# Optimization experiments

Hardware: AMD Instinct MI355X
Metric: run time of the kernel (lower is better)

The kernel has to match this reference:

```python
import jax, jax.numpy as jnp
import numpy as np

CH = 512
RED = CH // 8  # 64


def setup_inputs() -> dict:
    key = jax.random.key(0)
    ks = jax.random.split(key, 8)
    s = 0.05
    x = jax.random.normal(ks[0], (4, CH, 64, 64), dtype=jnp.float32)
    Wq = jax.random.normal(ks[1], (RED, CH), dtype=jnp.float32) * s
    bq = jnp.zeros((RED,), dtype=jnp.float32)
    Wk = jax.random.normal(ks[2], (RED, CH), dtype=jnp.float32) * s
    bk = jnp.zeros((RED,), dtype=jnp.float32)
    Wv = jax.random.normal(ks[3], (CH, CH), dtype=jnp.float32) * s
    bv = jnp.zeros((CH,), dtype=jnp.float32)
    gamma = jnp.zeros((1,), dtype=jnp.float32)
    return {"x": x, "Wq": Wq, "bq": bq, "Wk": Wk, "bk": bk, "Wv": Wv, "bv": bv, "gamma": gamma}


def reference(x, Wq, bq, Wk, bk, Wv, bv, gamma):
    b, c, h, w = x.shape
    n = h * w
    xf = x.reshape(b, c, n)  # [b, c, n]
    # 1x1 convs == per-pixel linear over channels
    q = jnp.einsum('rc,bcn->bnr', Wq, xf) + bq[None, None, :]   # [b, n, red]
    k = jnp.einsum('rc,bcn->brn', Wk, xf) + bk[None, :, None]   # [b, red, n]
    v = jnp.einsum('oc,bcn->bon', Wv, xf) + bv[None, :, None]   # [b, c, n]
    energy = jnp.einsum('bnr,brm->bnm', q, k)                   # [b, n, n]
    attention = jax.nn.softmax(energy, axis=-1)
    # out[b,c,i] = sum_j v[b,c,j] * attention[b,i,j]
    out = jnp.einsum('bcj,bij->bci', v, attention).reshape(b, c, h, w)
    return gamma[0] * out + x
```

## Files before the change

### kernel.cpp

```cpp
#include <hip/hip_runtime.h>
#include <math.h>

#define CH 512
#define RED 64

typedef __attribute__((ext_vector_type(4))) float f32x4;
typedef long i64;

typedef const __attribute__((address_space(1))) void* gas_t;
typedef __attribute__((address_space(3))) void* las_t;

static __device__ __forceinline__ void gl16(const void* g, void* l) {
    __builtin_amdgcn_global_load_lds((gas_t)g, (las_t)l, 16, 0, 0);
}

static __device__ __forceinline__ unsigned pk4(float a, float b, float c, float d) {
    int w = __builtin_amdgcn_cvt_pk_fp8_f32(a, b, 0, false);
    w = __builtin_amdgcn_cvt_pk_fp8_f32(c, d, w, true);
    return (unsigned)w;
}
static __device__ __forceinline__ unsigned char pk1(float a) {
    return (unsigned char)(__builtin_amdgcn_cvt_pk_fp8_f32(a, a, 0, false) & 0xFF);
}

__global__ __launch_bounds__(128) void prep_w(
    const float* __restrict__ Wq, const float* __restrict__ Wk,
    const float* __restrict__ Wv, unsigned char* __restrict__ Wcat)
{
    const int r = blockIdx.x, t = threadIdx.x;
    const float* src = (r < 64) ? (Wq + (size_t)r * CH)
                     : (r < 128) ? (Wk + (size_t)(r - 64) * CH)
                                 : (Wv + (size_t)(r - 128) * CH);
    const float4 v = *(const float4*)&src[t * 4];
    *(unsigned*)&Wcat[(size_t)r * CH + t * 4] = pk4(v.x, v.y, v.z, v.w);
}

__global__ __launch_bounds__(256) void cast_xt(
    const float* __restrict__ x, unsigned char* __restrict__ xT, int n)
{
    __shared__ float sX[64][65];
    const int b = blockIdx.z, i0 = blockIdx.x * 64, c0 = blockIdx.y * 64;
    const int t = threadIdx.x;
    #pragma unroll
    for (int s = 0; s < 4; ++s) {
        const int id = s * 256 + t, c = id >> 4, seg = id & 15;
        *(float4*)&sX[c][seg * 4] = *(const float4*)&x[((size_t)b * CH + c0 + c) * n + i0 + seg * 4];
    }
    __syncthreads();
    const int i = t >> 2, cp = t & 3;
    uint4 w;
    w.x = pk4(sX[cp*16+ 0][i], sX[cp*16+ 1][i], sX[cp*16+ 2][i], sX[cp*16+ 3][i]);
    w.y = pk4(sX[cp*16+ 4][i], sX[cp*16+ 5][i], sX[cp*16+ 6][i], sX[cp*16+ 7][i]);
    w.z = pk4(sX[cp*16+ 8][i], sX[cp*16+ 9][i], sX[cp*16+10][i], sX[cp*16+11][i]);
    w.w = pk4(sX[cp*16+12][i], sX[cp*16+13][i], sX[cp*16+14][i], sX[cp*16+15][i]);
    *(uint4*)&xT[((size_t)b * n + i0 + i) * CH + c0 + cp * 16] = w;
}

__global__ __launch_bounds__(256, 4) void qkv_gemm(
    const unsigned char* __restrict__ xT, const unsigned char* __restrict__ Wcat,
    const float* __restrict__ bq, const float* __restrict__ bk,
    const float* __restrict__ bv,
    unsigned char* __restrict__ qF, unsigned char* __restrict__ kF,
    unsigned char* __restrict__ v2, int n)
{
    __shared__ char smem[20480];
    const int b = blockIdx.z, i0 = blockIdx.x * 128, o0 = blockIdx.y * 128;
    const int t = threadIdx.x, lane = t & 63;
    const int quad = lane >> 4, l16 = lane & 15;
    const int wrow = (t >> 6) & 1, wcol = t >> 7;

    f32x4 acc[4][4];
    const f32x4 zz = {0.f, 0.f, 0.f, 0.f};
    #pragma unroll
    for (int mi = 0; mi < 4; ++mi)
        #pragma unroll
        for (int ci = 0; ci < 4; ++ci) acc[mi][ci] = zz;

    const unsigned char* Ab = xT + ((size_t)b * n + i0) * CH;
    const unsigned char* Bb = Wcat + (size_t)o0 * CH;

    for (int c0 = 0; c0 < CH; c0 += 64) {
        #pragma unroll
        for (int s = 0; s < 5; ++s) {
            const int c = s * 256 + t;
            const bool isA = c < 640;
            const int tc = isA ? c : c - 640;
            const int r = tc / 5, p = (tc % 5) & 3;
            gl16((isA ? Ab : Bb) + (size_t)r * CH + c0 + p * 16,
                 smem + (isA ? 0 : 10240) + (size_t)tc * 16);
        }
        __syncthreads();
        #pragma unroll
        for (int kk = 0; kk < 64; kk += 32) {
            i64 af[4], bf[4];
            #pragma unroll
            for (int mi = 0; mi < 4; ++mi)
                af[mi] = *(const i64*)(smem + (wrow * 64 + mi * 16 + l16) * 80 + kk + quad * 8);
            #pragma unroll
            for (int ci = 0; ci < 4; ++ci)
                bf[ci] = *(const i64*)(smem + 10240 + (wcol * 64 + ci * 16 + l16) * 80 + kk + quad * 8);
            #pragma unroll
            for (int mi = 0; mi < 4; ++mi)
                #pragma unroll
                for (int ci = 0; ci < 4; ++ci)
                    acc[mi][ci] = __builtin_amdgcn_mfma_f32_16x16x32_fp8_fp8(af[mi], bf[ci], acc[mi][ci], 0, 0, 0);
        }
        __syncthreads();
    }

    float bb[4];
    #pragma unroll
    for (int ci = 0; ci < 4; ++ci) {
        const int o = wcol * 64 + ci * 16 + l16;
        bb[ci] = (o0 == 0) ? ((o < 64) ? bq[o] : bk[o - 64]) : bv[o0 - 128 + o];
    }
    __syncthreads();
    unsigned char* sE = (unsigned char*)smem;
    if (o0 == 0) {
        #pragma unroll
        for (int mi = 0; mi < 4; ++mi)
            #pragma unroll
            for (int ci = 0; ci < 4; ++ci)
                #pragma unroll
                for (int r = 0; r < 4; ++r)
                    sE[(wrow*64 + mi*16 + quad*4 + r) * 144 + wcol*64 + ci*16 + l16] =
                        pk1(acc[mi][ci][r] + bb[ci]);
    } else {
        #pragma unroll
        for (int mi = 0; mi < 4; ++mi)
            #pragma unroll
            for (int ci = 0; ci < 4; ++ci)
                #pragma unroll
                for (int r = 0; r < 4; ++r)
                    sE[(wcol*64 + ci*16 + l16) * 144 + wrow*64 + mi*16 + quad*4 + r] =
                        pk1(acc[mi][ci][r] + bb[ci]);
    }
    __syncthreads();
    if (o0 == 0) {
        #pragma unroll
        for (int u = 0; u < 2; ++u) {
            const int id = u * 256 + t, i = id >> 2, p = id & 3;
            *(uint4*)&qF[((size_t)b * n + i0 + i) * RED + p * 16] = *(const uint4*)&sE[i * 144 + p * 16];
        }
        #pragma unroll
        for (int u = 0; u < 2; ++u) {
            const int id = u * 256 + t, i = id >> 2, p = id & 3;
            *(uint4*)&kF[((size_t)b * n + i0 + i) * RED + p * 16] = *(const uint4*)&sE[i * 144 + 64 + p * 16];
        }
    } else {
        #pragma unroll
        for (int u = 0; u < 4; ++u) {
            const int id = u * 256 + t, o = id >> 3, p = id & 7;
            *(uint4*)&v2[((size_t)b * CH + (o0 - 128) + o) * n + i0 + p * 16] =
                *(const uint4*)&sE[o * 144 + p * 16];
        }
    }
}

__global__ __launch_bounds__(256, 4) void rowmax(
    const unsigned char* __restrict__ qF, const unsigned char* __restrict__ kF,
    unsigned* __restrict__ mKey, int n)
{
    __shared__ char smem[20480];
    const int b = blockIdx.z, i0 = blockIdx.y * 128, j0 = blockIdx.x * 128;
    const int t = threadIdx.x, lane = t & 63;
    const int quad = lane >> 4, l16 = lane & 15;
    const int wrow = (t >> 6) & 1, wcol = t >> 7;

    const unsigned char* Qb = qF + ((size_t)b * n + i0) * RED;
    const unsigned char* Kb = kF + ((size_t)b * n + j0) * RED;
    #pragma unroll
    for (int s = 0; s < 5; ++s) {
        const int c = s * 256 + t;
        const bool isQ = c < 640;
        const int tc = isQ ? c : c - 640;
        const int r = tc / 5, p = (tc % 5) & 3;
        gl16((isQ ? Qb : Kb) + (size_t)r * RED + p * 16,
             smem + (isQ ? 0 : 10240) + (size_t)tc * 16);
    }
    __syncthreads();

    f32x4 acc[4][4];
    const f32x4 zz = {0.f, 0.f, 0.f, 0.f};
    #pragma unroll
    for (int mi = 0; mi < 4; ++mi)
        #pragma unroll
        for (int ci = 0; ci < 4; ++ci) acc[mi][ci] = zz;

    #pragma unroll
    for (int kk = 0; kk < 64; kk += 32) {
        i64 af[4], bf[4];
        #pragma unroll
        for (int mi = 0; mi < 4; ++mi)
            af[mi] = *(const i64*)(smem + (wrow * 64 + mi * 16 + l16) * 80 + kk + quad * 8);
        #pragma unroll
        for (int ci = 0; ci < 4; ++ci)
            bf[ci] = *(const i64*)(smem + 10240 + (wcol * 64 + ci * 16 + l16) * 80 + kk + quad * 8);
        #pragma unroll
        for (int mi = 0; mi < 4; ++mi)
            #pragma unroll
            for (int ci = 0; ci < 4; ++ci)
                acc[mi][ci] = __builtin_amdgcn_mfma_f32_16x16x32_fp8_fp8(af[mi], bf[ci], acc[mi][ci], 0, 0, 0);
    }

    #pragma unroll
    for (int mi = 0; mi < 4; ++mi)
        #pragma unroll
        for (int r = 0; r < 4; ++r) {
            float mx = fmaxf(fmaxf(acc[mi][0][r], acc[mi][1][r]),
                             fmaxf(acc[mi][2][r], acc[mi][3][r]));
            #pragma unroll
            for (int off = 1; off < 16; off <<= 1) mx = fmaxf(mx, __shfl_xor(mx, off));
            if (l16 == 0) {
                union { float f; unsigned u; } cv; cv.f = mx;
                const unsigned key = ((int)cv.u >= 0) ? (cv.u + 0x80000000u) : ~cv.u;
                atomicMax(&mKey[(size_t)b * n + i0 + wrow * 64 + mi * 16 + quad * 4 + r], key);
            }
        }
}

#define STGSZ 12288
#define SPOFF 24576
#define SLOFF 32768

__global__ __launch_bounds__(512, 4) void attn(
    const unsigned char* __restrict__ qF,
    const unsigned char* __restrict__ kF,
    const unsigned char* __restrict__ v2,
    const unsigned* __restrict__ mKey,
    const float* __restrict__ x, const float* __restrict__ gamma,
    float* __restrict__ y, int n)
{
    __shared__ char smem[34816];
    const int combo = blockIdx.x, it = blockIdx.y;
    const int b = combo >> 2, ch0 = (combo & 3) * 128;
    const int i0 = it * 128;
    const int t = threadIdx.x, lane = t & 63, w = t >> 6;
    const int quad = lane >> 4, l16 = lane & 15;
    const int qh = w & 1, g = w >> 1;
    const int sw = (l16 >> 1) & 3;
    const int boff = (quad & 1) * 8;
    const int phalf = quad >> 1;

    const unsigned char* Qb = qF + ((size_t)b * n + i0) * RED;
    const unsigned char* Kb = kF + (size_t)b * n * RED;
    const unsigned char* Vb = v2 + ((size_t)b * CH + ch0) * n;

    {
        const int r = t >> 2, s = t & 3, gs = s ^ ((r >> 1) & 3);
        gl16(Qb + (size_t)r * RED + gs * 16, smem + SPOFF + (size_t)t * 16);
        if (t < 256) {
            const int kr = t >> 2, ks = t & 3, kgs = ks ^ ((kr >> 1) & 3);
            gl16(Kb + (size_t)kr * RED + kgs * 16, smem + (size_t)t * 16);
        }
        gl16(Vb + (size_t)r * n + gs * 16, smem + 4096 + (size_t)t * 16);
    }
    __syncthreads();

    i64 qreg[4][2];
    #pragma unroll
    for (int qt = 0; qt < 4; ++qt) {
        const int row = qh * 64 + qt * 16 + l16;
        #pragma unroll
        for (int kki = 0; kki < 2; ++kki) {
            const int p = (kki * 2 + phalf) ^ sw;
            qreg[qt][kki] = *(const i64*)(smem + SPOFF + row * 64 + p * 16 + boff);
        }
    }
    float mrow[4];
    #pragma unroll
    for (int qt = 0; qt < 4; ++qt) {
        const unsigned u = mKey[(size_t)b * n + i0 + qh * 64 + qt * 16 + l16];
        const unsigned bits = (u >= 0x80000000u) ? (u - 0x80000000u) : ~u;
        union { unsigned u; float f; } cv; cv.u = bits;
        mrow[qt] = cv.f;
    }

    f32x4 acc[4][2];
    const f32x4 zz = {0.f, 0.f, 0.f, 0.f};
    #pragma unroll
    for (int qt = 0; qt < 4; ++qt) { acc[qt][0] = zz; acc[qt][1] = zz; }
    float lacc[4] = {0.f, 0.f, 0.f, 0.f};

    const int nchunks = n >> 6;
    for (int c = 0; c < nchunks; ++c) {
        const int j0 = c << 6;
        char* cur = smem + (c & 1) * STGSZ;
        char* nxt = smem + ((c & 1) ^ 1) * STGSZ;

        __syncthreads();
        if (j0 + 64 < n) {
            const int jn = j0 + 64;
            const int r = t >> 2, s = t & 3, gs = s ^ ((r >> 1) & 3);
            if (t < 256)
                gl16(Kb + (size_t)(jn + r) * RED + gs * 16, nxt + (size_t)t * 16);
            gl16(Vb + (size_t)r * n + jn + gs * 16, nxt + 4096 + (size_t)t * 16);
        }

        f32x4 S[4];
        #pragma unroll
        for (int qt = 0; qt < 4; ++qt) S[qt] = zz;
        #pragma unroll
        for (int kki = 0; kki < 2; ++kki) {
            const int p = (kki * 2 + phalf) ^ sw;
            const i64 kf = *(const i64*)(cur + (g * 16 + l16) * 64 + p * 16 + boff);
            #pragma unroll
            for (int qt = 0; qt < 4; ++qt)
                S[qt] = __builtin_amdgcn_mfma_f32_16x16x32_fp8_fp8(kf, qreg[qt][kki], S[qt], 0, 0, 0);
        }
        #pragma unroll
        for (int qt = 0; qt < 4; ++qt) {
            const float e0 = __expf(S[qt][0] - mrow[qt]);
            const float e1 = __expf(S[qt][1] - mrow[qt]);
            const float e2 = __expf(S[qt][2] - mrow[qt]);
            const float e3 = __expf(S[qt][3] - mrow[qt]);
            lacc[qt] += (e0 + e1) + (e2 + e3);
            const int qrow = qh * 64 + qt * 16 + l16;
            const int pp = g ^ sw;
            *(unsigned*)(smem + SPOFF + qrow * 64 + pp * 16 + quad * 4) = pk4(e0, e1, e2, e3);
        }
        __syncthreads();

        #pragma unroll
        for (int kki = 0; kki < 2; ++kki) {
            const int p = (kki * 2 + phalf) ^ sw;
            i64 vf[2], pf[4];
            #pragma unroll
            for (int ct = 0; ct < 2; ++ct) {
                const int row = (g * 2 + ct) * 16 + l16;
                vf[ct] = *(const i64*)(cur + 4096 + row * 64 + p * 16 + boff);
            }
            #pragma unroll
            for (int qt = 0; qt < 4; ++qt) {
                const int qrow = qh * 64 + qt * 16 + l16;
                pf[qt] = *(const i64*)(smem + SPOFF + qrow * 64 + p * 16 + boff);
            }
            #pragma unroll
            for (int qt = 0; qt < 4; ++qt)
                #pragma unroll
                for (int ct = 0; ct < 2; ++ct)
                    acc[qt][ct] = __builtin_amdgcn_mfma_f32_16x16x32_fp8_fp8(vf[ct], pf[qt], acc[qt][ct], 0, 0, 0);
        }
    }

    float* sL = (float*)(smem + SLOFF);
    #pragma unroll
    for (int qt = 0; qt < 4; ++qt) {
        float v = lacc[qt];
        v += __shfl_xor(v, 16);
        v += __shfl_xor(v, 32);
        lacc[qt] = v;
    }
    if (quad == 0) {
        #pragma unroll
        for (int qt = 0; qt < 4; ++qt) sL[w * 64 + qt * 16 + l16] = lacc[qt];
    }
    __syncthreads();
    float il[4];
    #pragma unroll
    for (int qt = 0; qt < 4; ++qt) {
        const int idx = qt * 16 + l16;
        il[qt] = 1.0f / (sL[qh * 64 + idx] + sL[(2 + qh) * 64 + idx] +
                         sL[(4 + qh) * 64 + idx] + sL[(6 + qh) * 64 + idx]);
    }

    const float gm = gamma[0];
    float* sT = (float*)smem;
    #pragma unroll
    for (int cr = 0; cr < 4; ++cr) {
        __syncthreads();
        if (g == cr) {
            #pragma unroll
            for (int ct = 0; ct < 2; ++ct)
                #pragma unroll
                for (int qt = 0; qt < 4; ++qt)
                    #pragma unroll
                    for (int r = 0; r < 4; ++r)
                        sT[(ct * 16 + quad * 4 + r) * 132 + qh * 64 + qt * 16 + l16] =
                            acc[qt][ct][r] * il[qt];
        }
        __syncthreads();
        const int row = t >> 4, seg = (t & 15) * 8;
        const size_t gb = ((size_t)b * CH + ch0 + cr * 32 + row) * n + i0 + seg;
        #pragma unroll
        for (int u = 0; u < 2; ++u) {
            const float4 xv = *(const float4*)&x[gb + u * 4];
            const float* op = &sT[row * 132 + seg + u * 4];
            float4 yv;
            yv.x = gm * op[0] + xv.x;
            yv.y = gm * op[1] + xv.y;
            yv.z = gm * op[2] + xv.z;
            yv.w = gm * op[3] + xv.w;
            *(float4*)&y[gb + u * 4] = yv;
        }
    }
}

extern "C" void kernel_launch(void* const* d_in, const int* in_sizes, int n_in,
                              void* d_out, int out_size, void* d_ws, size_t ws_size,
                              hipStream_t stream) {
    const float* x     = (const float*)d_in[0];
    const float* Wq    = (const float*)d_in[1];
    const float* bq    = (const float*)d_in[2];
    const float* Wk    = (const float*)d_in[3];
    const float* bk    = (const float*)d_in[4];
    const float* Wv    = (const float*)d_in[5];
    const float* bv    = (const float*)d_in[6];
    const float* gamma = (const float*)d_in[7];
    float* y = (float*)d_out;

    const int N = 64 * 64;
    const int B = in_sizes[0] / (CH * N);

    char* ws = (char*)d_ws;
    unsigned char* xT   = (unsigned char*)ws;  ws += (size_t)B * N * CH;
    unsigned char* qF   = (unsigned char*)ws;  ws += (size_t)B * N * RED;
    unsigned char* kF   = (unsigned char*)ws;  ws += (size_t)B * N * RED;
    unsigned char* v2   = (unsigned char*)ws;  ws += (size_t)B * CH * N;
    unsigned char* Wcat = (unsigned char*)ws;  ws += (size_t)640 * CH;
    unsigned* mKey      = (unsigned*)ws;

    hipMemsetAsync(mKey, 0, (size_t)B * N * 4, stream);

    prep_w<<<dim3(640), 128, 0, stream>>>(Wq, Wk, Wv, Wcat);
    cast_xt<<<dim3(N / 64, CH / 64, B), 256, 0, stream>>>(x, xT, N);
    qkv_gemm<<<dim3(N / 128, 5, B), 256, 0, stream>>>(xT, Wcat, bq, bk, bv, qF, kF, v2, N);
    rowmax<<<dim3(N / 128, N / 128, B), 256, 0, stream>>>(qF, kF, mKey, N);
    attn<<<dim3(4 * B, N / 128), 512, 0, stream>>>(qF, kF, v2, mKey, x, gamma, y, N);
}
```

Measured before the change: 253.1 us.

## Retile attention to 64 queries x 256 channels and fold log2e into Q

The attention kernel now gives each block 64 query rows and 256 output channels instead of 128x128. Each warp holds 2 query tiles and 4 channel tiles, and the staging buffers grow to hold twice as much V per chunk. This cuts the redundant QK^T and softmax work that was repeated across the four channel groups down to two groups. Q is pre-scaled by log2(e) in the projection so the softmax can use the hardware exp2 directly. The risk is that larger shared memory and more accumulators may lower occupancy, and fp8 rounding of the scaled Q slightly changes numerics.

```diff
diff --git a/kernel.cpp b/kernel.cpp
--- a/kernel.cpp
+++ b/kernel.cpp
@@ -21,6 +21,14 @@
 }
 static __device__ __forceinline__ unsigned char pk1(float a) {
     return (unsigned char)(__builtin_amdgcn_cvt_pk_fp8_f32(a, a, 0, false) & 0xFF);
+}
+
+static __device__ __forceinline__ float fexp2(float v) {
+#if __has_builtin(__builtin_amdgcn_exp2f)
+    return __builtin_amdgcn_exp2f(v);
+#else
+    float r; asm("v_exp_f32 %0, %1" : "=v"(r) : "v"(v)); return r;
+#endif
 }
 
 __global__ __launch_bounds__(128) void prep_w(
@@ -108,11 +116,17 @@
         __syncthreads();
     }
 
-    float bb[4];
+    float bb[4], scl[4];
     #pragma unroll
     for (int ci = 0; ci < 4; ++ci) {
         const int o = wcol * 64 + ci * 16 + l16;
-        bb[ci] = (o0 == 0) ? ((o < 64) ? bq[o] : bk[o - 64]) : bv[o0 - 128 + o];
+        if (o0 == 0) {
+            bb[ci]  = (o < 64) ? bq[o] : bk[o - 64];
+            scl[ci] = (o < 64) ? 1.44269504088896f : 1.0f;
+        } else {
+            bb[ci]  = bv[o0 - 128 + o];
+            scl[ci] = 1.0f;
+        }
     }
     __syncthreads();
     unsigned char* sE = (unsigned char*)smem;
@@ -124,7 +138,7 @@
                 #pragma unroll
                 for (int r = 0; r < 4; ++r)
                     sE[(wrow*64 + mi*16 + quad*4 + r) * 144 + wcol*64 + ci*16 + l16] =
-                        pk1(acc[mi][ci][r] + bb[ci]);
+                        pk1((acc[mi][ci][r] + bb[ci]) * scl[ci]);
     } else {
         #pragma unroll
         for (int mi = 0; mi < 4; ++mi)
@@ -219,9 +233,9 @@
         }
 }
 
-#define STGSZ 12288
-#define SPOFF 24576
-#define SLOFF 32768
+#define STGSZ 20480
+#define SPOFF 40960
+#define SLOFF 45056
 
 __global__ __launch_bounds__(512, 4) void attn(
     const unsigned char* __restrict__ qF,
@@ -231,10 +245,9 @@
     const float* __restrict__ x, const float* __restrict__ gamma,
     float* __restrict__ y, int n)
 {
-    __shared__ char smem[34816];
-    const int combo = blockIdx.x, it = blockIdx.y;
-    const int b = combo >> 2, ch0 = (combo & 3) * 128;
-    const int i0 = it * 128;
+    __shared__ char smem[46080];
+    const int b = blockIdx.x >> 1, ch0 = (blockIdx.x & 1) * 256;
+    const int i0 = blockIdx.y * 64;
     const int t = threadIdx.x, lane = t & 63, w = t >> 6;
     const int quad = lane >> 4, l16 = lane & 15;
     const int qh = w & 1, g = w >> 1;
@@ -248,39 +261,45 @@
 
     {
         const int r = t >> 2, s = t & 3, gs = s ^ ((r >> 1) & 3);
-        gl16(Qb + (size_t)r * RED + gs * 16, smem + SPOFF + (size_t)t * 16);
         if (t < 256) {
-            const int kr = t >> 2, ks = t & 3, kgs = ks ^ ((kr >> 1) & 3);
-            gl16(Kb + (size_t)kr * RED + kgs * 16, smem + (size_t)t * 16);
-        }
-        gl16(Vb + (size_t)r * n + gs * 16, smem + 4096 + (size_t)t * 16);
-    }
-    __syncthreads();
-
-    i64 qreg[4][2];
-    #pragma unroll
-    for (int qt = 0; qt < 4; ++qt) {
-        const int row = qh * 64 + qt * 16 + l16;
+            gl16(Qb + (size_t)r * RED + gs * 16, smem + SPOFF + (size_t)t * 16);
+            gl16(Kb + (size_t)r * RED + gs * 16, smem + (size_t)t * 16);
+        }
+        #pragma unroll
+        for (int ps = 0; ps < 2; ++ps) {
+            const int id = ps * 512 + t, vr = id >> 2, vs = id & 3;
+            const int vgs = vs ^ ((vr >> 1) & 3);
+            gl16(Vb + (size_t)vr * n + vgs * 16, smem + 4096 + (size_t)id * 16);
+        }
+    }
+    __syncthreads();
+
+    i64 qreg[2][2];
+    #pragma unroll
+    for (int qt = 0; qt < 2; ++qt) {
+        const int row = qh * 32 + qt * 16 + l16;
         #pragma unroll
         for (int kki = 0; kki < 2; ++kki) {
             const int p = (kki * 2 + phalf) ^ sw;
             qreg[qt][kki] = *(const i64*)(smem + SPOFF + row * 64 + p * 16 + boff);
         }
     }
-    float mrow[4];
-    #pragma unroll
-    for (int qt = 0; qt < 4; ++qt) {
-        const unsigned u = mKey[(size_t)b * n + i0 + qh * 64 + qt * 16 + l16];
+    float mrow[2];
+    #pragma unroll
+    for (int qt = 0; qt < 2; ++qt) {
+        const unsigned u = mKey[(size_t)b * n + i0 + qh * 32 + qt * 16 + l16];
         const unsigned bits = (u >= 0x80000000u) ? (u - 0x80000000u) : ~u;
         union { unsigned u; float f; } cv; cv.u = bits;
         mrow[qt] = cv.f;
     }
 
-    f32x4 acc[4][2];
+    f32x4 acc[2][4];
     const f32x4 zz = {0.f, 0.f, 0.f, 0.f};
     #pragma unroll
-    for (int qt = 0; qt < 4; ++qt) { acc[qt][0] = zz; acc[qt][1] = zz; }
-    float lacc[4] = {0.f, 0.f, 0.f, 0.f};
+    for (int qt = 0; qt < 2; ++qt)
+        #pragma unroll
+        for (int ct = 0; ct < 4; ++ct) acc[qt][ct] = zz;
+    float lacc[2] = {0.f, 0.f};
 
     const int nchunks = n >> 6;
     for (int c = 0; c < nchunks; ++c) {
@@ -294,28 +313,32 @@
             const int r = t >> 2, s = t & 3, gs = s ^ ((r >> 1) & 3);
             if (t < 256)
                 gl16(Kb + (size_t)(jn + r) * RED + gs * 16, nxt + (size_t)t * 16);
-            gl16(Vb + (size_t)r * n + jn + gs * 16, nxt + 4096 + (size_t)t * 16);
-        }
-
-        f32x4 S[4];
-        #pragma unroll
-        for (int qt = 0; qt < 4; ++qt) S[qt] = zz;
+            #pragma unroll
+            for (int ps = 0; ps < 2; ++ps) {
+                const int id = ps * 512 + t, vr = id >> 2, vs = id & 3;
+                const int vgs = vs ^ ((vr >> 1) & 3);
+                gl16(Vb + (size_t)vr * n + jn + vgs * 16, nxt + 4096 + (size_t)id * 16);
+            }
+        }
+
+        f32x4 S[2];
+        S[0] = zz; S[1] = zz;
         #pragma unroll
         for (int kki = 0; kki < 2; ++kki) {
             const int p = (kki * 2 + phalf) ^ sw;
             const i64 kf = *(const i64*)(cur + (g * 16 + l16) * 64 + p * 16 + boff);
             #pragma unroll
-            for (int qt = 0; qt < 4; ++qt)
+            for (int qt = 0; qt < 2; ++qt)
                 S[qt] = __builtin_amdgcn_mfma_f32_16x16x32_fp8_fp8(kf, qreg[qt][kki], S[qt], 0, 0, 0);
         }
         #pragma unroll
-        for (int qt = 0; qt < 4; ++qt) {
-            const float e0 = __expf(S[qt][0] - mrow[qt]);
-            const float e1 = __expf(S[qt][1] - mrow[qt]);
-            const float e2 = __expf(S[qt][2] - mrow[qt]);
-            const float e3 = __expf(S[qt][3] - mrow[qt]);
+        for (int qt = 0; qt < 2; ++qt) {
+            const float e0 = fexp2(S[qt][0] - mrow[qt]);
+            const float e1 = fexp2(S[qt][1] - mrow[qt]);
+            const float e2 = fexp2(S[qt][2] - mrow[qt]);
+            const float e3 = fexp2(S[qt][3] - mrow[qt]);
             lacc[qt] += (e0 + e1) + (e2 + e3);
-            const int qrow = qh * 64 + qt * 16 + l16;
+            const int qrow = qh * 32 + qt * 16 + l16;
             const int pp = g ^ sw;
             *(unsigned*)(smem + SPOFF + qrow * 64 + pp * 16 + quad * 4) = pk4(e0, e1, e2, e3);
         }
@@ -324,28 +347,28 @@
         #pragma unroll
         for (int kki = 0; kki < 2; ++kki) {
             const int p = (kki * 2 + phalf) ^ sw;
-            i64 vf[2], pf[4];
-            #pragma unroll
-            for (int ct = 0; ct < 2; ++ct) {
-                const int row = (g * 2 + ct) * 16 + l16;
+            i64 vf[4], pf[2];
+            #pragma unroll
+            for (int ct = 0; ct < 4; ++ct) {
+                const int row = g * 64 + ct * 16 + l16;
                 vf[ct] = *(const i64*)(cur + 4096 + row * 64 + p * 16 + boff);
             }
             #pragma unroll
-            for (int qt = 0; qt < 4; ++qt) {
-                const int qrow = qh * 64 + qt * 16 + l16;
+            for (int qt = 0; qt < 2; ++qt) {
+                const int qrow = qh * 32 + qt * 16 + l16;
                 pf[qt] = *(const i64*)(smem + SPOFF + qrow * 64 + p * 16 + boff);
             }
             #pragma unroll
-            for (int qt = 0; qt < 4; ++qt)
+            for (int qt = 0; qt < 2; ++qt)
                 #pragma unroll
-                for (int ct = 0; ct < 2; ++ct)
+                for (int ct = 0; ct < 4; ++ct)
                     acc[qt][ct] = __builtin_amdgcn_mfma_f32_16x16x32_fp8_fp8(vf[ct], pf[qt], acc[qt][ct], 0, 0, 0);
         }
     }
 
     float* sL = (float*)(smem + SLOFF);
     #pragma unroll
-    for (int qt = 0; qt < 4; ++qt) {
+    for (int qt = 0; qt < 2; ++qt) {
         float v = lacc[qt];
         v += __shfl_xor(v, 16);
         v += __shfl_xor(v, 32);
@@ -353,15 +376,15 @@
     }
     if (quad == 0) {
         #pragma unroll
-        for (int qt = 0; qt < 4; ++qt) sL[w * 64 + qt * 16 + l16] = lacc[qt];
-    }
-    __syncthreads();
-    float il[4];
-    #pragma unroll
-    for (int qt = 0; qt < 4; ++qt) {
+        for (int qt = 0; qt < 2; ++qt) sL[w * 32 + qt * 16 + l16] = lacc[qt];
+    }
+    __syncthreads();
+    float il[2];
+    #pragma unroll
+    for (int qt = 0; qt < 2; ++qt) {
         const int idx = qt * 16 + l16;
-        il[qt] = 1.0f / (sL[qh * 64 + idx] + sL[(2 + qh) * 64 + idx] +
-                         sL[(4 + qh) * 64 + idx] + sL[(6 + qh) * 64 + idx]);
+        il[qt] = 1.0f / (sL[qh * 32 + idx] + sL[(2 + qh) * 32 + idx] +
+                         sL[(4 + qh) * 32 + idx] + sL[(6 + qh) * 32 + idx]);
     }
 
     const float gm = gamma[0];
@@ -371,21 +394,21 @@
         __syncthreads();
         if (g == cr) {
             #pragma unroll
-            for (int ct = 0; ct < 2; ++ct)
+            for (int ct = 0; ct < 4; ++ct)
                 #pragma unroll
-                for (int qt = 0; qt < 4; ++qt)
+                for (int qt = 0; qt < 2; ++qt)
                     #pragma unroll
                     for (int r = 0; r < 4; ++r)
-                        sT[(ct * 16 + quad * 4 + r) * 132 + qh * 64 + qt * 16 + l16] =
+                        sT[(ct * 16 + quad * 4 + r) * 68 + qh * 32 + qt * 16 + l16] =
                             acc[qt][ct][r] * il[qt];
         }
         __syncthreads();
-        const int row = t >> 4, seg = (t & 15) * 8;
-        const size_t gb = ((size_t)b * CH + ch0 + cr * 32 + row) * n + i0 + seg;
+        const int row = t >> 3, seg = (t & 7) * 8;
+        const size_t gb = ((size_t)b * CH + ch0 + cr * 64 + row) * n + i0 + seg;
         #pragma unroll
         for (int u = 0; u < 2; ++u) {
             const float4 xv = *(const float4*)&x[gb + u * 4];
-            const float* op = &sT[row * 132 + seg + u * 4];
+            const float* op = &sT[row * 68 + seg + u * 4];
             float4 yv;
             yv.x = gm * op[0] + xv.x;
             yv.y = gm * op[1] + xv.y;
@@ -426,5 +449,5 @@
     cast_xt<<<dim3(N / 64, CH / 64, B), 256, 0, stream>>>(x, xT, N);
     qkv_gemm<<<dim3(N / 128, 5, B), 256, 0, stream>>>(xT, Wcat, bq, bk, bv, qF, kF, v2, N);
     rowmax<<<dim3(N / 128, N / 128, B), 256, 0, stream>>>(qF, kF, mKey, N);
-    attn<<<dim3(4 * B, N / 128), 512, 0, stream>>>(qF, kF, v2, mKey, x, gamma, y, N);
-}
+    attn<<<dim3(2 * B, N / 64), 512, 0, stream>>>(qF, kF, v2, mKey, x, gamma, y, N);
+}
```

Measured after the change: 219.3 us. -13.4%, faster.
